# Kernel optimization log

Measured on AMD Instinct MI355X. Metric: run time of the kernel, lower is better.

Reference implementation:

```python
import jax, jax.numpy as jnp
import numpy as np

HID = 512
HEADS = 8
HD = HID // HEADS  # 64


def setup_inputs() -> dict:
    key = jax.random.key(0)
    ks = jax.random.split(key, 16)
    B, LQ, LK = 2, 384, 384
    s_in = 1.0 / np.sqrt(HID)
    s_hd = 1.0 / np.sqrt(HD)
    return {
        "query": jax.random.normal(ks[0], (B, LQ, HID), jnp.float32),
        "key":   jax.random.normal(ks[1], (B, LK, HID), jnp.float32),
        "value": jax.random.normal(ks[2], (B, LK, HID), jnp.float32),
        # linear weights stored as (in, out) so y = x @ W + b
        "Wq": jax.random.uniform(ks[3], (HID, HID), jnp.float32, -s_in, s_in),
        "bq": jnp.zeros((HID,), jnp.float32),
        "Wk": jax.random.uniform(ks[4], (HID, HID), jnp.float32, -s_in, s_in),
        "bk": jnp.zeros((HID,), jnp.float32),
        "Wv": jax.random.uniform(ks[5], (HID, HID), jnp.float32, -s_in, s_in),
        "bv": jnp.zeros((HID,), jnp.float32),
        "Ww": jax.random.uniform(ks[6], (HD, HD), jnp.float32, -s_hd, s_hd),
        "bw": jnp.zeros((HD,), jnp.float32),
        "Wu": jax.random.uniform(ks[7], (HD, HD), jnp.float32, -s_hd, s_hd),
        "bu": jnp.zeros((HD,), jnp.float32),
        "vv": jax.random.uniform(ks[8], (HD,), jnp.float32, -s_hd, s_hd),
        "Wo": jax.random.uniform(ks[9], (HID, HID), jnp.float32, -s_in, s_in),
        "bo": jnp.zeros((HID,), jnp.float32),
    }


def reference(query, key, value, Wq, bq, Wk, bk, Wv, bv, Ww, bw, Wu, bu, vv, Wo, bo):
    B, LQ, _ = query.shape
    LK = key.shape[1]
    scale = jnp.sqrt(jnp.asarray(HD, query.dtype))

    def split_heads(x, L):
        return x.reshape(B, L, HEADS, HD).transpose(0, 2, 1, 3)  # [B,H,L,hd]

    Q = split_heads(query @ Wq + bq, LQ)
    K = split_heads(key @ Wk + bk, LK)
    V = split_heads(value @ Wv + bv, LK)

    qW = Q @ Ww + bw            # [B,H,Lq,hd]
    kU = K @ Wu + bu            # [B,H,Lk,hd]
    # additive energy: tanh(W(Q)+U(K)) . vv  -> [B,H,Lq,Lk]
    e = jnp.tanh(qW[:, :, :, None, :] + kU[:, :, None, :, :])  # [B,H,Lq,Lk,hd]
    energy = jnp.einsum('bhqkd,d->bhqk', e, vv) / scale

    attention = jax.nn.softmax(energy, axis=-1)
    x = jnp.einsum('bhqk,bhkd->bhqd', attention, V)
    x = x.transpose(0, 2, 1, 3).reshape(B, LQ, HID)
    x = x @ Wo + bo
    return (x, attention)
```

## Files before the change

### kernel.cpp

```cpp
#include <hip/hip_runtime.h>

#define HID 512
#define HEADS 8
#define HD 64
#define BATCH 2
#define SEQ 384
#define MROWS (BATCH * SEQ)
#define APACK_S8 (48 * 32 * 64)
#define BPACK_S8 (32 * 32 * 64)

#define C1 2.8853900817779268f
#define SSCL 0.18033688011112043f

typedef __attribute__((ext_vector_type(8))) short s8v;
typedef __attribute__((ext_vector_type(4))) float f4v;

__device__ __forceinline__ unsigned short bf16_rne(float x) {
    union { float f; unsigned u; } v; v.f = x;
    unsigned r = v.u + 0x7FFFu + ((v.u >> 16) & 1u);
    return (unsigned short)(r >> 16);
}
__device__ __forceinline__ float bf16_val(unsigned short h) {
    union { float f; unsigned u; } v; v.u = ((unsigned)h) << 16; return v.f;
}

__device__ __forceinline__ void pack_a_one(const float* __restrict__ src,
                                           s8v* __restrict__ dst, int rem)
{
    int g = rem & 63, m = rem >> 6;
    const float4* sp = (const float4*)(src + (size_t)m * HID + g * 8);
    float4 v0 = sp[0], v1 = sp[1];
    float vals[8] = {v0.x, v0.y, v0.z, v0.w, v1.x, v1.y, v1.z, v1.w};
    s8v hi, lo;
    #pragma unroll
    for (int j = 0; j < 8; ++j) {
        unsigned short h = bf16_rne(vals[j]);
        hi[j] = (short)h;
        lo[j] = (short)bf16_rne(vals[j] - bf16_val(h));
    }
    int mt = m >> 4, kt = g >> 2;
    int lanei = (m & 15) | ((g & 3) << 4);
    size_t base = ((size_t)mt * 32) * 64 + lanei;
    dst[base + (size_t)kt * 64]        = hi;
    dst[base + (size_t)(16 + kt) * 64] = lo;
}

__device__ __forceinline__ void pack_w_store(s8v* __restrict__ dst,
                                             const float vals[8], int kg, int n)
{
    s8v hi, lo;
    #pragma unroll
    for (int j = 0; j < 8; ++j) {
        unsigned short h = bf16_rne(vals[j]);
        hi[j] = (short)h;
        lo[j] = (short)bf16_rne(vals[j] - bf16_val(h));
    }
    int nt = n >> 4, kt = kg >> 2;
    int lanei = (n & 15) | ((kg & 3) << 4);
    size_t base = ((size_t)nt * 32) * 64 + lanei;
    dst[base + (size_t)kt * 64]        = hi;
    dst[base + (size_t)(16 + kt) * 64] = lo;
}

__device__ __forceinline__ void pack_w_one(const float* __restrict__ W,
                                           s8v* __restrict__ dst, int rem)
{
    int kg = rem >> 9, n = rem & 511;
    float vals[8];
    #pragma unroll
    for (int j = 0; j < 8; ++j)
        vals[j] = W[(size_t)(kg * 8 + j) * HID + n];
    pack_w_store(dst, vals, kg, n);
}

__device__ __forceinline__ void fold_pack_w_one(const float* __restrict__ Wbig,
                                                const float* __restrict__ Wsmall,
                                                s8v* __restrict__ dst, int rem)
{
    int kg = __builtin_amdgcn_readfirstlane(rem >> 9);
    int n  = rem & 511;
    int h  = __builtin_amdgcn_readfirstlane(n >> 6);
    int d  = n & 63;
    const float* wr = Wbig + (size_t)(kg * 8) * HID + h * HD;
    float acc[8] = {0.f, 0.f, 0.f, 0.f, 0.f, 0.f, 0.f, 0.f};
    #pragma unroll 8
    for (int t = 0; t < 64; ++t) {
        float wv = Wsmall[t * 64 + d];
        #pragma unroll
        for (int j = 0; j < 8; ++j)
            acc[j] = fmaf(wr[(size_t)j * HID + t], wv, acc[j]);
    }
    pack_w_store(dst, acc, kg, n);
}

__global__ __launch_bounds__(256) void pack_all_kernel(
    const float* __restrict__ q, const float* __restrict__ k, const float* __restrict__ v,
    const float* __restrict__ Wq, const float* __restrict__ bq,
    const float* __restrict__ Wk, const float* __restrict__ bk,
    const float* __restrict__ Wv, const float* __restrict__ Wo,
    const float* __restrict__ Ww, const float* __restrict__ bw,
    const float* __restrict__ Wu, const float* __restrict__ bu,
    const float* __restrict__ vv,
    s8v* __restrict__ Aq, s8v* __restrict__ Ak, s8v* __restrict__ Av,
    s8v* __restrict__ Bq, s8v* __restrict__ Bk, s8v* __restrict__ Bv, s8v* __restrict__ Bo,
    float* __restrict__ bqe, float* __restrict__ bke, float* __restrict__ vv2)
{
    int bx = blockIdx.x, tid = threadIdx.x;
    if (bx < 576) {
        int p = bx / 192;
        int rem = (bx % 192) * 256 + tid;
        const float* src = (p == 0) ? q : (p == 1) ? k : v;
        s8v* dst = (p == 0) ? Aq : (p == 1) ? Ak : Av;
        pack_a_one(src, dst, rem);
    } else if (bx < 704) {
        pack_w_one(Wv, Bv, (bx - 576) * 256 + tid);
    } else if (bx < 832) {
        pack_w_one(Wo, Bo, (bx - 704) * 256 + tid);
    } else if (bx < 960) {
        fold_pack_w_one(Wq, Ww, Bq, (bx - 832) * 256 + tid);
    } else if (bx < 1088) {
        fold_pack_w_one(Wk, Wu, Bk, (bx - 960) * 256 + tid);
    } else {
        for (int i = tid; i < 1088; i += 256) {
            if (i < 512) {
                int h = i >> 6, j = i & 63;
                float s = bw[j];
                for (int t = 0; t < 64; ++t) s = fmaf(bq[h * 64 + t], Ww[t * 64 + j], s);
                bqe[i] = s;
            } else if (i < 1024) {
                int n = i - 512, h = n >> 6, j = n & 63;
                float s = bu[j];
                for (int t = 0; t < 64; ++t) s = fmaf(bk[h * 64 + t], Wu[t * 64 + j], s);
                bke[n] = s;
            } else {
                vv2[i - 1024] = -2.0f * vv[i - 1024];
            }
        }
    }
}

struct Frag { s8v ah0, al0, ah1, al1, bh0, bl0, bh1, bl1; };

__device__ __forceinline__ void load_frag(Frag& f,
    const s8v* __restrict__ a0, const s8v* __restrict__ a1,
    const s8v* __restrict__ b0, const s8v* __restrict__ b1, int kt)
{
    int oh = kt * 64, ol = (16 + kt) * 64;
    f.ah0 = a0[oh]; f.al0 = a0[ol];
    f.ah1 = a1[oh]; f.al1 = a1[ol];
    f.bh0 = b0[oh]; f.bl0 = b0[ol];
    f.bh1 = b1[oh]; f.bl1 = b1[ol];
}

__device__ __forceinline__ void compute_frag(f4v& acc00, f4v& acc01,
                                             f4v& acc10, f4v& acc11, const Frag& f)
{
    acc00 = __builtin_amdgcn_mfma_f32_16x16x32_bf16(f.ah0, f.bh0, acc00, 0, 0, 0);
    acc01 = __builtin_amdgcn_mfma_f32_16x16x32_bf16(f.ah0, f.bh1, acc01, 0, 0, 0);
    acc10 = __builtin_amdgcn_mfma_f32_16x16x32_bf16(f.ah1, f.bh0, acc10, 0, 0, 0);
    acc11 = __builtin_amdgcn_mfma_f32_16x16x32_bf16(f.ah1, f.bh1, acc11, 0, 0, 0);
    acc00 = __builtin_amdgcn_mfma_f32_16x16x32_bf16(f.ah0, f.bl0, acc00, 0, 0, 0);
    acc01 = __builtin_amdgcn_mfma_f32_16x16x32_bf16(f.ah0, f.bl1, acc01, 0, 0, 0);
    acc10 = __builtin_amdgcn_mfma_f32_16x16x32_bf16(f.ah1, f.bl0, acc10, 0, 0, 0);
    acc11 = __builtin_amdgcn_mfma_f32_16x16x32_bf16(f.ah1, f.bl1, acc11, 0, 0, 0);
    acc00 = __builtin_amdgcn_mfma_f32_16x16x32_bf16(f.al0, f.bh0, acc00, 0, 0, 0);
    acc01 = __builtin_amdgcn_mfma_f32_16x16x32_bf16(f.al0, f.bh1, acc01, 0, 0, 0);
    acc10 = __builtin_amdgcn_mfma_f32_16x16x32_bf16(f.al1, f.bh0, acc10, 0, 0, 0);
    acc11 = __builtin_amdgcn_mfma_f32_16x16x32_bf16(f.al1, f.bh1, acc11, 0, 0, 0);
}

template <int MODE>
__device__ __forceinline__ void mfma_gemm_body(
    const s8v* __restrict__ Ap, const s8v* __restrict__ Bp,
    const float* __restrict__ bias, float* __restrict__ out,
    int mt0, int nt0)
{
    int lane = threadIdx.x & 63;

    const s8v* a0p = Ap + (size_t)(mt0 * 32) * 64 + lane;
    const s8v* a1p = a0p + (size_t)32 * 64;
    const s8v* b0p = Bp + (size_t)(nt0 * 32) * 64 + lane;
    const s8v* b1p = b0p + (size_t)32 * 64;

    f4v acc00 = {0.f, 0.f, 0.f, 0.f};
    f4v acc01 = {0.f, 0.f, 0.f, 0.f};
    f4v acc10 = {0.f, 0.f, 0.f, 0.f};
    f4v acc11 = {0.f, 0.f, 0.f, 0.f};

    Frag X, Y;
    load_frag(X, a0p, a1p, b0p, b1p, 0);
    #pragma unroll 1
    for (int kt = 0; kt < 16; kt += 2) {
        load_frag(Y, a0p, a1p, b0p, b1p, kt + 1);
        compute_frag(acc00, acc01, acc10, acc11, X);
        load_frag(X, a0p, a1p, b0p, b1p, (kt + 2) & 15);
        compute_frag(acc00, acc01, acc10, acc11, Y);
    }

    int quad = lane >> 4, c16 = lane & 15;
    int col0 = nt0 * 16 + c16, col1 = col0 + 16;
    float bias0 = bias[col0], bias1 = bias[col1];
    int row0 = mt0 * 16 + quad * 4;
    int row1 = row0 + 16;

    #pragma unroll
    for (int r = 0; r < 4; ++r) {
        float y;
        #define WR(ROW, COL, Y)                                                     \
        {                                                                           \
            float yy = (Y);                                                         \
            if (MODE != 0) yy = __builtin_amdgcn_exp2f(C1 * yy);                    \
            if (MODE == 2) {                                                        \
                int b2 = (ROW) / SEQ, kk = (ROW) - b2 * SEQ;                        \
                int hh = (COL) >> 6, dd = (COL) & 63;                               \
                out[(((size_t)((b2 * 8 + hh) * 16 + (dd >> 2)) * SEQ + kk) << 2)    \
                    + (dd & 3)] = yy;                                               \
            } else {                                                                \
                out[(size_t)(ROW) * HID + (COL)] = yy;                              \
            }                                                                       \
        }
        y = acc00[r] + bias0; WR(row0 + r, col0, y);
        y = acc01[r] + bias1; WR(row0 + r, col1, y);
        y = acc10[r] + bias0; WR(row1 + r, col0, y);
        y = acc11[r] + bias1; WR(row1 + r, col1, y);
        #undef WR
    }
}

__global__ __launch_bounds__(64) void proj3_mfma_kernel(
    const s8v* __restrict__ Aq, const s8v* __restrict__ Ak, const s8v* __restrict__ Av,
    const s8v* __restrict__ Bq, const s8v* __restrict__ Bk, const s8v* __restrict__ Bv,
    const float* __restrict__ bqe, const float* __restrict__ bke, const float* __restrict__ bv,
    float* __restrict__ Eq, float* __restrict__ Ek4, float* __restrict__ V)
{
    int p = blockIdx.z;
    int mt0 = blockIdx.x * 2, nt0 = blockIdx.y * 2;
    if (p == 0)      mfma_gemm_body<1>(Aq, Bq, bqe, Eq,  mt0, nt0);
    else if (p == 1) mfma_gemm_body<2>(Ak, Bk, bke, Ek4, mt0, nt0);
    else             mfma_gemm_body<0>(Av, Bv, bv,  V,   mt0, nt0);
}

__global__ __launch_bounds__(64) void out_mfma_kernel(
    const s8v* __restrict__ Ax, const s8v* __restrict__ Bo,
    const float* __restrict__ bo, float* __restrict__ out)
{
    mfma_gemm_body<0>(Ax, Bo, bo, out, blockIdx.x * 2, blockIdx.y * 2);
}

__global__ __launch_bounds__(256, 4) void attn_kernel(
    const float* __restrict__ Eq, const float* __restrict__ Ek4,
    const float* __restrict__ V, const float* __restrict__ vv2,
    float* __restrict__ attnOut, s8v* __restrict__ Ax)
{
    __shared__ float2 aP[4][SEQ];

    int blk = blockIdx.x;
    int xcd = blk & 7, slot = blk >> 3;
    int part = slot / 48, qblk = slot % 48;
    int bh = xcd * 2 + part;
    int b = bh >> 3, h = bh & 7;
    int tid = threadIdx.x;
    int wave = __builtin_amdgcn_readfirstlane(tid >> 6);
    int lane = tid & 63;
    int q0 = qblk * 8 + wave * 2, q1 = q0 + 1;

    const float* eq0 = Eq + (size_t)(b * SEQ + q0) * HID + h * HD;
    const float* eq1 = eq0 + HID;
    const float4* ekbase = (const float4*)Ek4 + (size_t)bh * 16 * SEQ + lane;

    float e0[6], e1[6];
    #pragma unroll
    for (int t = 0; t < 6; ++t) { e0[t] = 0.f; e1[t] = 0.f; }

    #pragma unroll 1
    for (int cc = 0; cc < 4; ++cc) {
        int c = (cc + wave) & 3;
        float g0[16], g1[16], w[16];
        #pragma unroll
        for (int j = 0; j < 16; ++j) {
            g0[j] = eq0[c * 16 + j];
            g1[j] = eq1[c * 16 + j];
            w[j]  = vv2[c * 16 + j];
        }
        const float4* ekc = ekbase + (size_t)c * 4 * SEQ;
        float4 k0 = ekc[0 * SEQ], k1 = ekc[1 * SEQ];
        float4 k2 = ekc[2 * SEQ], k3 = ekc[3 * SEQ];
        #pragma unroll
        for (int kt = 0; kt < 6; ++kt) {
            float4 n0, n1, n2, n3;
            if (kt < 5) {
                const float4* np = ekc + (kt + 1) * 64;
                n0 = np[0 * SEQ]; n1 = np[1 * SEQ];
                n2 = np[2 * SEQ]; n3 = np[3 * SEQ];
            }
            float r0 = e0[kt], r1 = e1[kt];
            #define EN(J, KV)                                                      \
            {                                                                      \
                float t0 = __builtin_amdgcn_rcpf(fmaf(g0[J], (KV), 1.f));          \
                float t1 = __builtin_amdgcn_rcpf(fmaf(g1[J], (KV), 1.f));          \
                r0 = fmaf(w[J], t0, r0);                                           \
                r1 = fmaf(w[J], t1, r1);                                           \
            }
            EN(0,  k0.x) EN(1,  k0.y) EN(2,  k0.z) EN(3,  k0.w)
            EN(4,  k1.x) EN(5,  k1.y) EN(6,  k1.z) EN(7,  k1.w)
            EN(8,  k2.x) EN(9,  k2.y) EN(10, k2.z) EN(11, k2.w)
            EN(12, k3.x) EN(13, k3.y) EN(14, k3.z) EN(15, k3.w)
            #undef EN
            e0[kt] = r0; e1[kt] = r1;
            k0 = n0; k1 = n1; k2 = n2; k3 = n3;
        }
    }

    int ko = lane >> 4, d4p = lane & 15;
    const float4* vb = (const float4*)&V[(size_t)b * SEQ * HID + h * HD + d4p * 4];
    float4 vpre[8];
    #pragma unroll
    for (int i = 0; i < 8; ++i)
        vpre[i] = vb[(size_t)(ko + i * 4) * (HID / 4)];

    float m0 = e0[0], m1 = e1[0];
    #pragma unroll
    for (int t = 1; t < 6; ++t) { m0 = fmaxf(m0, e0[t]); m1 = fmaxf(m1, e1[t]); }
    #pragma unroll
    for (int off = 1; off < 64; off <<= 1) {
        m0 = fmaxf(m0, __shfl_xor(m0, off));
        m1 = fmaxf(m1, __shfl_xor(m1, off));
    }
    float a0[6], a1[6], s0 = 0.f, s1 = 0.f;
    #pragma unroll
    for (int t = 0; t < 6; ++t) {
        a0[t] = __builtin_amdgcn_exp2f((e0[t] - m0) * SSCL); s0 += a0[t];
        a1[t] = __builtin_amdgcn_exp2f((e1[t] - m1) * SSCL); s1 += a1[t];
    }
    #pragma unroll
    for (int off = 1; off < 64; off <<= 1) {
        s0 += __shfl_xor(s0, off);
        s1 += __shfl_xor(s1, off);
    }
    float z0 = __builtin_amdgcn_rcpf(s0), z1 = __builtin_amdgcn_rcpf(s1);

    size_t abase = (size_t)bh * SEQ * SEQ + (size_t)q0 * SEQ;
    #pragma unroll
    for (int t = 0; t < 6; ++t) {
        float v0 = a0[t] * z0, v1 = a1[t] * z1;
        attnOut[abase + t * 64 + lane] = v0;
        attnOut[abase + SEQ + t * 64 + lane] = v1;
        aP[wave][t * 64 + lane] = make_float2(v0, v1);
    }

    float4 x0 = make_float4(0.f, 0.f, 0.f, 0.f);
    float4 x1 = make_float4(0.f, 0.f, 0.f, 0.f);
    #pragma unroll
    for (int i = 0; i < 8; ++i) {
        int k = ko + i * 4;
        float4 v = vpre[i];
        float2 a = aP[wave][k];
        x0.x = fmaf(a.x, v.x, x0.x); x0.y = fmaf(a.x, v.y, x0.y);
        x0.z = fmaf(a.x, v.z, x0.z); x0.w = fmaf(a.x, v.w, x0.w);
        x1.x = fmaf(a.y, v.x, x1.x); x1.y = fmaf(a.y, v.y, x1.y);
        x1.z = fmaf(a.y, v.z, x1.z); x1.w = fmaf(a.y, v.w, x1.w);
    }
    #pragma unroll 8
    for (int k = ko + 32; k < SEQ; k += 4) {
        float4 v = vb[(size_t)k * (HID / 4)];
        float2 a = aP[wave][k];
        x0.x = fmaf(a.x, v.x, x0.x); x0.y = fmaf(a.x, v.y, x0.y);
        x0.z = fmaf(a.x, v.z, x0.z); x0.w = fmaf(a.x, v.w, x0.w);
        x1.x = fmaf(a.y, v.x, x1.x); x1.y = fmaf(a.y, v.y, x1.y);
        x1.z = fmaf(a.y, v.z, x1.z); x1.w = fmaf(a.y, v.w, x1.w);
    }
    #pragma unroll
    for (int off = 16; off < 64; off <<= 1) {
        x0.x += __shfl_xor(x0.x, off); x0.y += __shfl_xor(x0.y, off);
        x0.z += __shfl_xor(x0.z, off); x0.w += __shfl_xor(x0.w, off);
        x1.x += __shfl_xor(x1.x, off); x1.y += __shfl_xor(x1.y, off);
        x1.z += __shfl_xor(x1.z, off); x1.w += __shfl_xor(x1.w, off);
    }

    if (ko == 0) {
        float4 p0, p1;
        p0.x = __shfl_xor(x0.x, 1); p0.y = __shfl_xor(x0.y, 1);
        p0.z = __shfl_xor(x0.z, 1); p0.w = __shfl_xor(x0.w, 1);
        p1.x = __shfl_xor(x1.x, 1); p1.y = __shfl_xor(x1.y, 1);
        p1.z = __shfl_xor(x1.z, 1); p1.w = __shfl_xor(x1.w, 1);
        float vals[8];
        int row;
        if ((lane & 1) == 0) {
            vals[0] = x0.x; vals[1] = x0.y; vals[2] = x0.z; vals[3] = x0.w;
            vals[4] = p0.x; vals[5] = p0.y; vals[6] = p0.z; vals[7] = p0.w;
            row = b * SEQ + q0;
        } else {
            vals[0] = p1.x; vals[1] = p1.y; vals[2] = p1.z; vals[3] = p1.w;
            vals[4] = x1.x; vals[5] = x1.y; vals[6] = x1.z; vals[7] = x1.w;
            row = b * SEQ + q1;
        }
        int g = h * 8 + (lane >> 1);
        s8v hi, lo;
        #pragma unroll
        for (int j = 0; j < 8; ++j) {
            unsigned short hh = bf16_rne(vals[j]);
            hi[j] = (short)hh;
            lo[j] = (short)bf16_rne(vals[j] - bf16_val(hh));
        }
        int mt = row >> 4, kt2 = g >> 2;
        int lanei = (row & 15) | ((g & 3) << 4);
        size_t base = ((size_t)mt * 32) * 64 + lanei;
        Ax[base + (size_t)kt2 * 64]        = hi;
        Ax[base + (size_t)(16 + kt2) * 64] = lo;
    }
}

extern "C" void kernel_launch(void* const* d_in, const int* in_sizes, int n_in,
                              void* d_out, int out_size, void* d_ws, size_t ws_size,
                              hipStream_t stream)
{
    const float* query = (const float*)d_in[0];
    const float* key   = (const float*)d_in[1];
    const float* value = (const float*)d_in[2];
    const float* Wq = (const float*)d_in[3];
    const float* bq = (const float*)d_in[4];
    const float* Wk = (const float*)d_in[5];
    const float* bk = (const float*)d_in[6];
    const float* Wv = (const float*)d_in[7];
    const float* bv = (const float*)d_in[8];
    const float* Ww = (const float*)d_in[9];
    const float* bw = (const float*)d_in[10];
    const float* Wu = (const float*)d_in[11];
    const float* bu = (const float*)d_in[12];
    const float* vv = (const float*)d_in[13];
    const float* Wo = (const float*)d_in[14];
    const float* bo = (const float*)d_in[15];

    float* out_x    = (float*)d_out;
    float* out_attn = out_x + (size_t)MROWS * HID;

    float* ws  = (float*)d_ws;
    float* bqe = ws;
    float* bke = bqe + 512;
    float* vv2 = bke + 512;
    float* EqB = vv2 + 64;
    float* Ek4 = EqB + 393216;
    float* Vw  = Ek4 + 393216;

    s8v* packs = (s8v*)(Vw + 393216);
    s8v* Aq = packs;
    s8v* Ak = Aq + APACK_S8;
    s8v* Av = Ak + APACK_S8;
    s8v* Ax = Av + APACK_S8;
    s8v* Bq = Ax + APACK_S8;
    s8v* Bk = Bq + BPACK_S8;
    s8v* Bv = Bk + BPACK_S8;
    s8v* Bo = Bv + BPACK_S8;

    pack_all_kernel<<<dim3(1089), 256, 0, stream>>>(
        query, key, value,
        Wq, bq, Wk, bk, Wv, Wo, Ww, bw, Wu, bu, vv,
        Aq, Ak, Av, Bq, Bk, Bv, Bo,
        bqe, bke, vv2);
    proj3_mfma_kernel<<<dim3(24, 16, 3), 64, 0, stream>>>(Aq, Ak, Av, Bq, Bk, Bv,
                                                          bqe, bke, bv,
                                                          EqB, Ek4, Vw);
    attn_kernel<<<dim3(768), 256, 0, stream>>>(EqB, Ek4, Vw, vv2, out_attn, Ax);
    out_mfma_kernel<<<dim3(24, 16), 64, 0, stream>>>(Ax, Bo, bo, out_x);
}
```

Before: 141.0 us.

## Split GEMM K dimension across four waves with LDS reduction

The projection and output GEMM blocks grow from one wave to four. Each wave handles a quarter of the K loop, and the partial accumulators are reduced through shared memory. Each wave then writes one 16x16 output quadrant. This gives four times the waves for latency hiding and a shorter serial K chain per wave, at the cost of an LDS round trip, a barrier and more wavefronts per block.

```diff
diff --git a/kernel.cpp b/kernel.cpp
--- a/kernel.cpp
+++ b/kernel.cpp
@@ -175,7 +175,11 @@
     const float* __restrict__ bias, float* __restrict__ out,
     int mt0, int nt0)
 {
-    int lane = threadIdx.x & 63;
+    __shared__ f4v red[4][4][64];
+
+    int tid  = threadIdx.x;
+    int wave = __builtin_amdgcn_readfirstlane(tid >> 6);
+    int lane = tid & 63;
 
     const s8v* a0p = Ap + (size_t)(mt0 * 32) * 64 + lane;
     const s8v* a1p = a0p + (size_t)32 * 64;
@@ -187,47 +191,48 @@
     f4v acc10 = {0.f, 0.f, 0.f, 0.f};
     f4v acc11 = {0.f, 0.f, 0.f, 0.f};
 
+    int kt0 = wave * 4;
     Frag X, Y;
-    load_frag(X, a0p, a1p, b0p, b1p, 0);
-    #pragma unroll 1
-    for (int kt = 0; kt < 16; kt += 2) {
-        load_frag(Y, a0p, a1p, b0p, b1p, kt + 1);
-        compute_frag(acc00, acc01, acc10, acc11, X);
-        load_frag(X, a0p, a1p, b0p, b1p, (kt + 2) & 15);
-        compute_frag(acc00, acc01, acc10, acc11, Y);
-    }
+    load_frag(X, a0p, a1p, b0p, b1p, kt0);
+    load_frag(Y, a0p, a1p, b0p, b1p, kt0 + 1);
+    compute_frag(acc00, acc01, acc10, acc11, X);
+    load_frag(X, a0p, a1p, b0p, b1p, kt0 + 2);
+    compute_frag(acc00, acc01, acc10, acc11, Y);
+    load_frag(Y, a0p, a1p, b0p, b1p, kt0 + 3);
+    compute_frag(acc00, acc01, acc10, acc11, X);
+    compute_frag(acc00, acc01, acc10, acc11, Y);
+
+    red[wave][0][lane] = acc00;
+    red[wave][1][lane] = acc01;
+    red[wave][2][lane] = acc10;
+    red[wave][3][lane] = acc11;
+    __syncthreads();
+
+    f4v s = red[0][wave][lane] + red[1][wave][lane]
+          + red[2][wave][lane] + red[3][wave][lane];
 
     int quad = lane >> 4, c16 = lane & 15;
-    int col0 = nt0 * 16 + c16, col1 = col0 + 16;
-    float bias0 = bias[col0], bias1 = bias[col1];
-    int row0 = mt0 * 16 + quad * 4;
-    int row1 = row0 + 16;
+    int R0 = mt0 * 16 + quad * 4 + (wave >> 1) * 16;
+    int C  = nt0 * 16 + c16 + (wave & 1) * 16;
+    float biasC = bias[C];
 
     #pragma unroll
     for (int r = 0; r < 4; ++r) {
-        float y;
-        #define WR(ROW, COL, Y)                                                     \
-        {                                                                           \
-            float yy = (Y);                                                         \
-            if (MODE != 0) yy = __builtin_amdgcn_exp2f(C1 * yy);                    \
-            if (MODE == 2) {                                                        \
-                int b2 = (ROW) / SEQ, kk = (ROW) - b2 * SEQ;                        \
-                int hh = (COL) >> 6, dd = (COL) & 63;                               \
-                out[(((size_t)((b2 * 8 + hh) * 16 + (dd >> 2)) * SEQ + kk) << 2)    \
-                    + (dd & 3)] = yy;                                               \
-            } else {                                                                \
-                out[(size_t)(ROW) * HID + (COL)] = yy;                              \
-            }                                                                       \
-        }
-        y = acc00[r] + bias0; WR(row0 + r, col0, y);
-        y = acc01[r] + bias1; WR(row0 + r, col1, y);
-        y = acc10[r] + bias0; WR(row1 + r, col0, y);
-        y = acc11[r] + bias1; WR(row1 + r, col1, y);
-        #undef WR
-    }
-}
-
-__global__ __launch_bounds__(64) void proj3_mfma_kernel(
+        float yy = s[r] + biasC;
+        if (MODE != 0) yy = __builtin_amdgcn_exp2f(C1 * yy);
+        if (MODE == 2) {
+            int ROW = R0 + r;
+            int b2 = ROW / SEQ, kk = ROW - b2 * SEQ;
+            int hh = C >> 6, dd = C & 63;
+            out[(((size_t)((b2 * 8 + hh) * 16 + (dd >> 2)) * SEQ + kk) << 2)
+                + (dd & 3)] = yy;
+        } else {
+            out[(size_t)(R0 + r) * HID + C] = yy;
+        }
+    }
+}
+
+__global__ __launch_bounds__(256) void proj3_mfma_kernel(
     const s8v* __restrict__ Aq, const s8v* __restrict__ Ak, const s8v* __restrict__ Av,
     const s8v* __restrict__ Bq, const s8v* __restrict__ Bk, const s8v* __restrict__ Bv,
     const float* __restrict__ bqe, const float* __restrict__ bke, const float* __restrict__ bv,
@@ -240,7 +245,7 @@
     else             mfma_gemm_body<0>(Av, Bv, bv,  V,   mt0, nt0);
 }
 
-__global__ __launch_bounds__(64) void out_mfma_kernel(
+__global__ __launch_bounds__(256) void out_mfma_kernel(
     const s8v* __restrict__ Ax, const s8v* __restrict__ Bo,
     const float* __restrict__ bo, float* __restrict__ out)
 {
@@ -457,9 +462,9 @@
         Wq, bq, Wk, bk, Wv, Wo, Ww, bw, Wu, bu, vv,
         Aq, Ak, Av, Bq, Bk, Bv, Bo,
         bqe, bke, vv2);
-    proj3_mfma_kernel<<<dim3(24, 16, 3), 64, 0, stream>>>(Aq, Ak, Av, Bq, Bk, Bv,
-                                                          bqe, bke, bv,
-                                                          EqB, Ek4, Vw);
+    proj3_mfma_kernel<<<dim3(24, 16, 3), 256, 0, stream>>>(Aq, Ak, Av, Bq, Bk, Bv,
+                                                           bqe, bke, bv,
+                                                           EqB, Ek4, Vw);
     attn_kernel<<<dim3(768), 256, 0, stream>>>(EqB, Ek4, Vw, vv2, out_attn, Ax);
-    out_mfma_kernel<<<dim3(24, 16), 64, 0, stream>>>(Ax, Bo, bo, out_x);
-}
+    out_mfma_kernel<<<dim3(24, 16), 256, 0, stream>>>(Ax, Bo, bo, out_x);
+}
```

Result: no change. 140.8 us, median of 2 (-0.2%).
